# Kernel tuning notes

Measured on AMD Instinct MI355X. Metric: run time of the kernel, lower is better.

The kernel has to match this reference:

```python
import jax, jax.numpy as jnp
import numpy as np

LN_EPS = 1e-12


def setup_inputs() -> dict:
    key = jax.random.key(0)
    ks = jax.random.split(key, 5)
    B, N, D_IN, D_OUT, E = 32, 2048, 128, 128, 64
    return {
        "x": jax.random.normal(ks[0], (B, N, D_IN), dtype=jnp.float32),
        "node_embeddings": jax.random.normal(ks[1], (N, E), dtype=jnp.float32),
        "time_embeddings": jax.random.normal(ks[2], (E,), dtype=jnp.float32),
        "weights_pool": jax.random.normal(ks[3], (E, 2, D_IN, D_OUT), dtype=jnp.float32) * 0.02,
        "bias_pool": jax.random.normal(ks[4], (E, D_OUT), dtype=jnp.float32) * 0.02,
        "ln_weight": jnp.ones((E,), dtype=jnp.float32),
        "ln_bias": jnp.zeros((E,), dtype=jnp.float32),
    }


def reference(x, node_embeddings, time_embeddings, weights_pool, bias_pool, ln_weight, ln_bias):
    # e: [N, E] = LayerNorm(node_emb + time_emb)  (dropout in eval mode = identity)
    e = node_embeddings + time_embeddings[None, :]
    mu = jnp.mean(e, axis=-1, keepdims=True)
    var = jnp.mean(jnp.square(e - mu), axis=-1, keepdims=True)
    e = (e - mu) * jax.lax.rsqrt(var + LN_EPS) * ln_weight + ln_bias

    # adaptive adjacency: softmax over rows of e @ e.T  -> [N, N]
    adj = jax.nn.softmax(jnp.einsum('nd,md->nm', e, e), axis=1)

    # per-node weights [N, 2, I, O] and bias [N, O]
    weights = jnp.einsum('nd,dkio->nkio', e, weights_pool)
    bias = e @ bias_pool  # [N, O]

    # supports: k=0 identity (x itself), k=1 adjacency aggregation
    x_agg = jnp.einsum('nm,bmc->bnc', adj, x)        # [B, N, I]
    x_g = jnp.stack([x, x_agg], axis=2)              # [B, N, 2, I]

    # per-node batched GEMM + bias
    out = jnp.einsum('bnki,nkio->bno', x_g, weights) + bias
    return out
```

## Files before the change

### kernel.cpp

```cpp
#include <hip/hip_runtime.h>


typedef unsigned short u16;
typedef unsigned int u32;
typedef __attribute__((ext_vector_type(8))) short bf16x8;
typedef __attribute__((ext_vector_type(4))) float f32x4;
typedef const __attribute__((address_space(1))) u16* gas1;
typedef __attribute__((address_space(3))) u16* las3;

#define NN 2048
#define EE 64
#define CC 128
#define BB 32

__device__ __forceinline__ u16 f2bf(float f) {
  u32 u = __builtin_bit_cast(u32, f);
  u += 0x7fffu + ((u >> 16) & 1u);
  return (u16)(u >> 16);
}

__device__ __forceinline__ f32x4 mfma16(bf16x8 a, bf16x8 b, f32x4 c) {
  return __builtin_amdgcn_mfma_f32_16x16x32_bf16(a, b, c, 0, 0, 0);
}

__global__ __launch_bounds__(256) void k_mega0(
    const float* __restrict__ x, const float* __restrict__ ne,
    const float* __restrict__ te, const float* __restrict__ pool,
    const float* __restrict__ bias_pool, const float* __restrict__ lnw,
    const float* __restrict__ lnb,
    float* __restrict__ e, u16* __restrict__ e_bf, float* __restrict__ bias_out,
    u16* __restrict__ pool_r, u16* __restrict__ x_t, u16* __restrict__ xg_t) {
  __shared__ __align__(16) char smem[33280];
  int bid = blockIdx.x;
  int tid = threadIdx.x;
  if (bid < 512) {
    float* sh = (float*)smem;
    int nw = tid >> 6, d = tid & 63;
    int n = bid * 4 + nw;
    float v = ne[n * EE + d] + te[d];
    float s = v;
#pragma unroll
    for (int off = 32; off > 0; off >>= 1) s += __shfl_xor(s, off);
    float mean = s * (1.0f / 64.0f);
    float c = v - mean;
    float q = c * c;
#pragma unroll
    for (int off = 32; off > 0; off >>= 1) q += __shfl_xor(q, off);
    float inv = rsqrtf(q * (1.0f / 64.0f) + 1e-12f);
    float ev = c * inv * lnw[d] + lnb[d];
    e[n * EE + d] = ev;
    e_bf[n * EE + d] = f2bf(ev);
    sh[nw * 64 + d] = ev;
    __syncthreads();
#pragma unroll
    for (int oo = 0; oo < 2; ++oo) {
      int o = oo * 64 + d;
      float acc = 0.f;
#pragma unroll 8
      for (int dd = 0; dd < 64; ++dd) acc += sh[nw * 64 + dd] * bias_pool[dd * CC + o];
      bias_out[n * CC + o] = acc;
    }
  } else if (bid < 768) {
    float* t = (float*)smem;
    int ki = bid - 512;
    for (int it = 0; it < 32; ++it) {
      int idx = it * 256 + tid;
      int d = idx >> 7, o = idx & 127;
      t[o * 65 + d] = pool[d * 32768 + ki * 128 + o];
    }
    __syncthreads();
    for (int it = 0; it < 32; ++it) {
      int idx = it * 256 + tid;
      int o = idx >> 6, d = idx & 63;
      pool_r[((size_t)o * 256 + ki) * 64 + d] = f2bf(t[o * 65 + d]);
    }
  } else {
    u16* t = (u16*)smem;
    int bx = bid - 768;
    int b = bx >> 5;
    int m0 = (bx & 31) * 64;
    for (int it = 0; it < 32; ++it) {
      int idx = it * 256 + tid;
      int m = idx >> 7, c = idx & 127;
      float v = x[((size_t)b * NN + m0 + m) * CC + c];
      t[c * 68 + m] = f2bf(v);
    }
    __syncthreads();
    for (int it = 0; it < 32; ++it) {
      int idx = it * 256 + tid;
      int c = idx >> 6, m = idx & 63;
      x_t[((size_t)b * CC + c) * NN + m0 + m] = t[c * 68 + m];
    }
    for (int it = 0; it < 16; ++it) {
      int idx = it * 256 + tid;
      int m = idx >> 6, c2 = idx & 63;
      float2 v = *(const float2*)&x[((size_t)b * NN + m0 + m) * CC + c2 * 2];
      u32 pk = (u32)f2bf(v.x) | ((u32)f2bf(v.y) << 16);
      *(u32*)&xg_t[(((size_t)(m0 + m)) * 32 + b) * 256 + c2 * 2] = pk;
    }
  }
}

__global__ __launch_bounds__(256) void k_Sexp(const float* __restrict__ e,
                                              u16* __restrict__ P,
                                              float* __restrict__ rs) {
  __shared__ float er[64 * 68];
  __shared__ float ec[64 * 68];
  int n0 = (blockIdx.x >> 5) * 64, m0 = (blockIdx.x & 31) * 64;
  int tid = threadIdx.x;
  for (int it = 0; it < 16; ++it) {
    int idx = it * 256 + tid;
    int r = idx >> 6, d = idx & 63;
    er[r * 68 + d] = e[(n0 + r) * EE + d];
    ec[r * 68 + d] = e[(m0 + r) * EE + d];
  }
  __syncthreads();
  int tx = tid & 15, ty = tid >> 4;
  float acc[4][4] = {};
  for (int d4 = 0; d4 < 64; d4 += 4) {
    f32x4 av[4], bv[4];
#pragma unroll
    for (int i = 0; i < 4; ++i) av[i] = *(const f32x4*)&er[(ty + 16 * i) * 68 + d4];
#pragma unroll
    for (int j = 0; j < 4; ++j) bv[j] = *(const f32x4*)&ec[(tx + 16 * j) * 68 + d4];
#pragma unroll
    for (int i = 0; i < 4; ++i)
#pragma unroll
      for (int j = 0; j < 4; ++j) {
        acc[i][j] += av[i][0] * bv[j][0];
        acc[i][j] += av[i][1] * bv[j][1];
        acc[i][j] += av[i][2] * bv[j][2];
        acc[i][j] += av[i][3] * bv[j][3];
      }
  }
#pragma unroll
  for (int i = 0; i < 4; ++i) {
    float s = 0.f;
#pragma unroll
    for (int j = 0; j < 4; ++j) {
      float pv = __expf(acc[i][j]);
      P[(size_t)(n0 + ty + 16 * i) * NN + m0 + tx + 16 * j] = f2bf(pv);
      s += pv;
    }
#pragma unroll
    for (int off = 8; off > 0; off >>= 1) s += __shfl_xor(s, off);
    if (tx == 0) atomicAdd(&rs[n0 + ty + 16 * i], s);
  }
}

__global__ __launch_bounds__(256, 4) void k_aggr(
    const u16* __restrict__ P, const u16* __restrict__ x_t,
    const float* __restrict__ rs, u16* __restrict__ xg_t) {
  __shared__ __align__(16) char smem[32768];
  int tid = threadIdx.x;
  int lane = tid & 63, w = tid >> 6;
  int lm = lane & 15, lq = lane >> 4;
  u16* As = (u16*)smem;
  u16* Bs = (u16*)(smem + 16384);
  int mb = blockIdx.x & 15, b = blockIdx.x >> 4;
  int n0 = mb * 128;
  int wm = w >> 1, wn = w & 1;
  f32x4 acc[4][4] = {};
  const u16* a_src = P + (size_t)n0 * NN;
  const u16* b_src = x_t + (size_t)b * CC * NN;
  for (int kc = 0; kc < NN; kc += 64) {
    __syncthreads();
#pragma unroll
    for (int ii = 0; ii < 4; ++ii) {
      int idx = ii * 256 + tid;
      int row = idx >> 3, ch = idx & 7;
      __builtin_amdgcn_global_load_lds((gas1)(a_src + (size_t)row * NN + kc + ch * 8),
                                       (las3)(As + (size_t)(ii * 256 + w * 64) * 8), 16, 0, 0);
      __builtin_amdgcn_global_load_lds((gas1)(b_src + (size_t)row * NN + kc + ch * 8),
                                       (las3)(Bs + (size_t)(ii * 256 + w * 64) * 8), 16, 0, 0);
    }
    __syncthreads();
#pragma unroll
    for (int kk = 0; kk < 64; kk += 32) {
      bf16x8 af[4], bq[4];
#pragma unroll
      for (int i = 0; i < 4; ++i)
        af[i] = *(const bf16x8*)&As[(wm * 64 + i * 16 + lm) * 64 + kk + lq * 8];
#pragma unroll
      for (int j = 0; j < 4; ++j)
        bq[j] = *(const bf16x8*)&Bs[(wn * 64 + j * 16 + lm) * 64 + kk + lq * 8];
#pragma unroll
      for (int i = 0; i < 4; ++i)
#pragma unroll
        for (int j = 0; j < 4; ++j)
          acc[i][j] = mfma16(af[i], bq[j], acc[i][j]);
    }
  }
#pragma unroll
  for (int i = 0; i < 4; ++i) {
    int nr = n0 + wm * 64 + i * 16 + lq * 4;
#pragma unroll
    for (int r = 0; r < 4; ++r) {
      float sc = 1.0f / rs[nr + r];
#pragma unroll
      for (int j = 0; j < 4; ++j) {
        int c = wn * 64 + j * 16 + lm;
        xg_t[((size_t)(nr + r) * 32 + b) * 256 + 128 + c] = f2bf(acc[i][j][r] * sc);
      }
    }
  }
}

#define GA_OS 40
#define GA_NS 648
__global__ __launch_bounds__(256) void k_genapply(
    const u16* __restrict__ e_bf, const u16* __restrict__ pool_r,
    const u16* __restrict__ xg_t, const float* __restrict__ biasb,
    float* __restrict__ out) {
  __shared__ u16 W[32 * GA_NS];
  int tid = threadIdx.x;
  int lane = tid & 63, w = tid >> 6;
  int lm = lane & 15, lq = lane >> 4;
  int ng = blockIdx.x & 63, og = blockIdx.x >> 6;
  int n0 = ng * 32, o0 = og * 16;

  bf16x8 eB[2][2];
#pragma unroll
  for (int nc = 0; nc < 2; ++nc)
#pragma unroll
    for (int ks = 0; ks < 2; ++ks)
      eB[nc][ks] = *(const bf16x8*)&e_bf[(n0 + nc * 16 + lm) * EE + ks * 32 + lq * 8];

  f32x4 acc[8][2] = {};
  for (int kt = 0; kt < 8; ++kt) {
    int ki0 = kt * 32;
    if (kt) __syncthreads();
#pragma unroll
    for (int ot = 0; ot < 4; ++ot) {
      int o_l = w * 4 + ot;
      const u16* pb = pool_r + ((size_t)(o0 + o_l) * 256 + ki0 + lm) * 64 + lq * 8;
#pragma unroll
      for (int kc = 0; kc < 2; ++kc) {
        const u16* ap = pb + kc * 16 * 64;
        bf16x8 a0 = *(const bf16x8*)ap;
        bf16x8 a1 = *(const bf16x8*)(ap + 32);
#pragma unroll
        for (int nc = 0; nc < 2; ++nc) {
          f32x4 d = {0.f, 0.f, 0.f, 0.f};
          d = mfma16(a0, eB[nc][0], d);
          d = mfma16(a1, eB[nc][1], d);
          ushort4 h;
          h.x = f2bf(d[0]); h.y = f2bf(d[1]); h.z = f2bf(d[2]); h.w = f2bf(d[3]);
          *(ushort4*)&W[(nc * 16 + lm) * GA_NS + o_l * GA_OS + kc * 16 + lq * 4] = h;
        }
      }
    }
    __syncthreads();
#pragma unroll
    for (int i = 0; i < 8; ++i) {
      int n_l = w * 8 + i;
      bf16x8 wA = *(const bf16x8*)&W[n_l * GA_NS + lm * GA_OS + lq * 8];
      const u16* xp = xg_t + ((size_t)(n0 + n_l) * 32) * 256 + ki0 + lq * 8;
      bf16x8 x0 = *(const bf16x8*)(xp + lm * 256);
      bf16x8 x1 = *(const bf16x8*)(xp + (16 + lm) * 256);
      acc[i][0] = mfma16(wA, x0, acc[i][0]);
      acc[i][1] = mfma16(wA, x1, acc[i][1]);
    }
  }
#pragma unroll
  for (int i = 0; i < 8; ++i) {
    int n = n0 + w * 8 + i;
    float4 bv = *(const float4*)&biasb[n * CC + o0 + lq * 4];
#pragma unroll
    for (int bt = 0; bt < 2; ++bt) {
      int b = bt * 16 + lm;
      float4 o4;
      o4.x = acc[i][bt][0] + bv.x;
      o4.y = acc[i][bt][1] + bv.y;
      o4.z = acc[i][bt][2] + bv.z;
      o4.w = acc[i][bt][3] + bv.w;
      *(float4*)&out[((size_t)b * NN + n) * CC + o0 + lq * 4] = o4;
    }
  }
}

extern "C" void kernel_launch(void* const* d_in, const int* in_sizes, int n_in,
                              void* d_out, int out_size, void* d_ws, size_t ws_size,
                              hipStream_t stream) {
  const float* x        = (const float*)d_in[0];
  const float* node_emb = (const float*)d_in[1];
  const float* time_emb = (const float*)d_in[2];
  const float* pool     = (const float*)d_in[3];
  const float* bias_pl  = (const float*)d_in[4];
  const float* ln_w     = (const float*)d_in[5];
  const float* ln_b     = (const float*)d_in[6];
  float* out = (float*)d_out;

  char* p = (char*)d_ws;
  auto alloc = [&](size_t bytes) {
    char* r = p;
    p += (bytes + 255) & ~(size_t)255;
    return r;
  };
  float* e      = (float*)alloc((size_t)NN * EE * 4);
  u16*   e_bf   = (u16*)  alloc((size_t)NN * EE * 2);
  float* biasb  = (float*)alloc((size_t)NN * CC * 4);
  u16*   Pm     = (u16*)  alloc((size_t)NN * NN * 2);
  float* rs     = (float*)alloc((size_t)NN * 4);
  u16*   x_t    = (u16*)  alloc((size_t)BB * CC * NN * 2);
  u16*   xg_t   = (u16*)  alloc((size_t)NN * BB * 256 * 2);
  u16*   pool_r = (u16*)  alloc((size_t)128 * 256 * 64 * 2);

  if (ws_size < (size_t)(p - (char*)d_ws)) return;

  (void)hipMemsetAsync(rs, 0, (size_t)NN * 4, stream);

  k_mega0<<<1792, 256, 0, stream>>>(x, node_emb, time_emb, pool, bias_pl, ln_w, ln_b,
                                    e, e_bf, biasb, pool_r, x_t, xg_t);
  k_Sexp<<<1024, 256, 0, stream>>>(e, Pm, rs);
  k_aggr<<<512, 256, 0, stream>>>(Pm, x_t, rs, xg_t);
  k_genapply<<<512, 256, 0, stream>>>(e_bf, pool_r, xg_t, biasb, out);
}
```

Baseline: 247.2 us.

## Double-buffer generated weights in genapply and halve node tile for more blocks

The weight-generation-plus-apply kernel now uses 16-node tiles instead of 32, doubling the grid to 1024 blocks. Generated per-node weights go into a double-buffered shared array, so generation for the next k-tile overlaps with the MFMAs on the current one, and one barrier per iteration replaces two. The LDS padding shrinks, weight reads are split into two 4-wide loads, and launch bounds now request 4 blocks per CU. Each block regenerates weights for fewer nodes, so the pool reads are shared across fewer nodes, which adds global traffic in exchange for more parallelism and overlap.

```diff
diff --git a/kernel.cpp b/kernel.cpp
--- a/kernel.cpp
+++ b/kernel.cpp
@@ -4,6 +4,7 @@
 typedef unsigned short u16;
 typedef unsigned int u32;
 typedef __attribute__((ext_vector_type(8))) short bf16x8;
+typedef __attribute__((ext_vector_type(4))) short bf16x4;
 typedef __attribute__((ext_vector_type(4))) float f32x4;
 typedef const __attribute__((address_space(1))) u16* gas1;
 typedef __attribute__((address_space(3))) u16* las3;
@@ -206,30 +207,27 @@
   }
 }
 
-#define GA_OS 40
-#define GA_NS 648
-__global__ __launch_bounds__(256) void k_genapply(
+#define GA_OS 36
+#define GA_NS 584
+__global__ __launch_bounds__(256, 4) void k_genapply(
     const u16* __restrict__ e_bf, const u16* __restrict__ pool_r,
     const u16* __restrict__ xg_t, const float* __restrict__ biasb,
     float* __restrict__ out) {
-  __shared__ u16 W[32 * GA_NS];
+  __shared__ u16 W[2][16 * GA_NS];
   int tid = threadIdx.x;
   int lane = tid & 63, w = tid >> 6;
   int lm = lane & 15, lq = lane >> 4;
-  int ng = blockIdx.x & 63, og = blockIdx.x >> 6;
-  int n0 = ng * 32, o0 = og * 16;
-
-  bf16x8 eB[2][2];
-#pragma unroll
-  for (int nc = 0; nc < 2; ++nc)
-#pragma unroll
-    for (int ks = 0; ks < 2; ++ks)
-      eB[nc][ks] = *(const bf16x8*)&e_bf[(n0 + nc * 16 + lm) * EE + ks * 32 + lq * 8];
-
-  f32x4 acc[8][2] = {};
-  for (int kt = 0; kt < 8; ++kt) {
+  int ng = blockIdx.x & 127, og = blockIdx.x >> 7;
+  int n0 = ng * 16, o0 = og * 16;
+
+  bf16x8 eB[2];
+#pragma unroll
+  for (int ks = 0; ks < 2; ++ks)
+    eB[ks] = *(const bf16x8*)&e_bf[(n0 + lm) * EE + ks * 32 + lq * 8];
+
+  auto GEN = [&](int kt) {
+    u16* Wb = &W[kt & 1][0];
     int ki0 = kt * 32;
-    if (kt) __syncthreads();
 #pragma unroll
     for (int ot = 0; ot < 4; ++ot) {
       int o_l = w * 4 + ot;
@@ -239,32 +237,48 @@
         const u16* ap = pb + kc * 16 * 64;
         bf16x8 a0 = *(const bf16x8*)ap;
         bf16x8 a1 = *(const bf16x8*)(ap + 32);
-#pragma unroll
-        for (int nc = 0; nc < 2; ++nc) {
-          f32x4 d = {0.f, 0.f, 0.f, 0.f};
-          d = mfma16(a0, eB[nc][0], d);
-          d = mfma16(a1, eB[nc][1], d);
-          ushort4 h;
-          h.x = f2bf(d[0]); h.y = f2bf(d[1]); h.z = f2bf(d[2]); h.w = f2bf(d[3]);
-          *(ushort4*)&W[(nc * 16 + lm) * GA_NS + o_l * GA_OS + kc * 16 + lq * 4] = h;
-        }
+        f32x4 d = {0.f, 0.f, 0.f, 0.f};
+        d = mfma16(a0, eB[0], d);
+        d = mfma16(a1, eB[1], d);
+        ushort4 h;
+        h.x = f2bf(d[0]); h.y = f2bf(d[1]); h.z = f2bf(d[2]); h.w = f2bf(d[3]);
+        *(ushort4*)&Wb[lm * GA_NS + o_l * GA_OS + kc * 16 + lq * 4] = h;
       }
     }
-    __syncthreads();
-#pragma unroll
-    for (int i = 0; i < 8; ++i) {
-      int n_l = w * 8 + i;
-      bf16x8 wA = *(const bf16x8*)&W[n_l * GA_NS + lm * GA_OS + lq * 8];
+  };
+
+  f32x4 acc[4][2] = {};
+  GEN(0);
+  __syncthreads();
+
+  for (int kt = 0; kt < 8; ++kt) {
+    int ki0 = kt * 32;
+    const u16* Wb = &W[kt & 1][0];
+    bf16x8 xv[4][2];
+    bf16x4 wlo[4], whi[4];
+#pragma unroll
+    for (int i = 0; i < 4; ++i) {
+      int n_l = w * 4 + i;
       const u16* xp = xg_t + ((size_t)(n0 + n_l) * 32) * 256 + ki0 + lq * 8;
-      bf16x8 x0 = *(const bf16x8*)(xp + lm * 256);
-      bf16x8 x1 = *(const bf16x8*)(xp + (16 + lm) * 256);
-      acc[i][0] = mfma16(wA, x0, acc[i][0]);
-      acc[i][1] = mfma16(wA, x1, acc[i][1]);
-    }
-  }
-#pragma unroll
-  for (int i = 0; i < 8; ++i) {
-    int n = n0 + w * 8 + i;
+      xv[i][0] = *(const bf16x8*)(xp + lm * 256);
+      xv[i][1] = *(const bf16x8*)(xp + (16 + lm) * 256);
+      const u16* wp = &Wb[n_l * GA_NS + lm * GA_OS + lq * 8];
+      wlo[i] = *(const bf16x4*)wp;
+      whi[i] = *(const bf16x4*)(wp + 4);
+    }
+    if (kt < 7) GEN(kt + 1);
+#pragma unroll
+    for (int i = 0; i < 4; ++i) {
+      bf16x8 wA = __builtin_shufflevector(wlo[i], whi[i], 0, 1, 2, 3, 4, 5, 6, 7);
+      acc[i][0] = mfma16(wA, xv[i][0], acc[i][0]);
+      acc[i][1] = mfma16(wA, xv[i][1], acc[i][1]);
+    }
+    __syncthreads();
+  }
+
+#pragma unroll
+  for (int i = 0; i < 4; ++i) {
+    int n = n0 + w * 4 + i;
     float4 bv = *(const float4*)&biasb[n * CC + o0 + lq * 4];
 #pragma unroll
     for (int bt = 0; bt < 2; ++bt) {
@@ -314,5 +328,5 @@
                                     e, e_bf, biasb, pool_r, x_t, xg_t);
   k_Sexp<<<1024, 256, 0, stream>>>(e, Pm, rs);
   k_aggr<<<512, 256, 0, stream>>>(Pm, x_t, rs, xg_t);
-  k_genapply<<<512, 256, 0, stream>>>(e_bf, pool_r, xg_t, biasb, out);
-}
+  k_genapply<<<1024, 256, 0, stream>>>(e_bf, pool_r, xg_t, biasb, out);
+}
```

Result: slower. 274.6 us (+11.1%).
